# Optimization experiments

Hardware: AMD Instinct MI355X
Metric: run time of the kernel (lower is better)

The kernel has to match this reference:

```python
import jax, jax.numpy as jnp
import numpy as np

N_QUBITS = 10
N_LAYERS = 2
OUT_FEATURES = 64
N_BATCH = 128


def _apply_ry(state, theta, q, n):
    # state: [B, 2^n] real (RY gates are real), theta: [B]
    B = state.shape[0]
    left = 2 ** q
    right = 2 ** (n - q - 1)
    s = state.reshape(B, left, 2, right)
    half = theta * 0.5
    c = jnp.cos(half)[:, None, None]
    sn = jnp.sin(half)[:, None, None]
    s0 = s[:, :, 0, :]
    s1 = s[:, :, 1, :]
    out = jnp.stack([c * s0 - sn * s1, sn * s0 + c * s1], axis=2)
    return out.reshape(B, -1)


def _apply_cnot(state, q, n):
    # control qubit q, target qubit q+1 (adjacent), real statevector
    B = state.shape[0]
    left = 2 ** q
    right = 2 ** (n - q - 2)
    s = state.reshape(B, left, 2, 2, right)
    flipped = jnp.flip(s[:, :, 1, :, :], axis=2)  # swap target amps where control=1
    out = jnp.stack([s[:, :, 0, :, :], flipped], axis=2)
    return out.reshape(B, -1)


def _zdiag(n):
    # diagonal of H = sum_i Z_i in the computational basis: n - 2*popcount(index)
    idx = np.arange(2 ** n)
    pop = np.array([bin(i).count('1') for i in range(2 ** n)], dtype=np.float32)
    return jnp.asarray(n - 2.0 * pop, dtype=jnp.float32)


def setup_inputs() -> dict:
    key = jax.random.key(0)
    kx, kw = jax.random.split(key)
    x = jax.random.normal(kx, (N_BATCH, N_QUBITS), dtype=jnp.float32)
    weight = jax.random.normal(kw, (OUT_FEATURES, N_QUBITS, N_LAYERS), dtype=jnp.float32)
    return {"x": x, "weight": weight}


def reference(x, weight):
    n_batch, n = x.shape
    out_features, _, n_layers = weight.shape
    B = out_features * n_batch
    # x.repeat(out_features, 1): tile batch across output features
    xb = jnp.tile(x, (out_features, 1))  # [B, n]
    # weight expanded over batch: [O, 1, n, L] -> [O, nb, n, L] -> [B, n, L]
    pb = jnp.broadcast_to(weight[:, None, :, :], (out_features, n_batch, n, n_layers))
    pb = pb.reshape(B, n, n_layers)
    # |0...0> statevector, real since the circuit (RY + CNOT) is real
    state = jnp.zeros((B, 2 ** n), dtype=jnp.float32).at[:, 0].set(1.0)
    # data-encoding layer: RY(x_q) on each qubit
    for q in range(n):
        state = _apply_ry(state, xb[:, q], q, n)
    # variational layers: RY(theta_{q,l}) on each qubit + CNOT ladder entangler
    for l in range(n_layers):
        for q in range(n):
            state = _apply_ry(state, pb[:, q, l], q, n)
        for q in range(n - 1):
            state = _apply_cnot(state, q, n)
    zd = _zdiag(n)
    # energy expectation <psi| sum_i Z_i |psi> (real circuit -> real output)
    out = jnp.einsum('bk,k->b', state * state, zd)  # [B]
    return out.reshape(out_features, n_batch)
```

## Files before the change

kernel.cpp:

```cpp
#include <hip/hip_runtime.h>
#include <math.h>


__global__ __launch_bounds__(128) void qnn_closed_v14(const float* gx,
                                                      const float* gw,
                                                      float* gout) {
    __shared__ float wc0[10], ws0[10], wc1[10], ws1[10];
    const int b = (int)threadIdx.x;
    const int f = (int)blockIdx.x;

    if (b < 20) {
        const int q = b % 10;
        const int l = b / 10;
        const float a = gw[(f * 10 + q) * 2 + l];
        if (l == 0) { wc0[q] = cosf(a); ws0[q] = sinf(a); }
        else        { wc1[q] = cosf(a); ws1[q] = sinf(a); }
    }
    __syncthreads();

    float z[10], xv[10], cc[10], ss[10];
    #pragma unroll
    for (int q = 0; q < 10; ++q) {
        const float xa = gx[b * 10 + q];
        const float cx = cosf(xa), sx = sinf(xa);
        z[q]  = cx * wc0[q] - sx * ws0[q];
        xv[q] = sx * wc0[q] + cx * ws0[q];
        cc[q] = wc1[q];
        ss[q] = ws1[q];
    }

    float E = 0.0f;
    #pragma unroll
    for (int k = 0; k < 10; ++k) {
        float v00 = cc[k];
        float v10 = -ss[k] * ((k < 9) ? xv[k + 1] : 1.0f);
        float v01 = 0.0f, v11 = 0.0f;
        #pragma unroll
        for (int j = k - 1; j >= 0; --j) {
            const float zj = z[j + 1], xj = xv[j + 1];
            const float n00 =  cc[j] * (v01 + xj * v10);
            const float n01 =  cc[j] * (zj * v00);
            const float n10 = -ss[j] * (xj * v01 + v10);
            const float n11 = -ss[j] * (zj * v11);
            v00 = n00; v01 = n01; v10 = n10; v11 = n11;
        }
        E += v00 * z[0] + v01 + v10 * xv[0];
    }

    gout[f * 128 + b] = E;
}

extern "C" void kernel_launch(void* const* d_in, const int* in_sizes, int n_in,
                              void* d_out, int out_size, void* d_ws, size_t ws_size,
                              hipStream_t stream) {
    const float* x = (const float*)d_in[0];
    const float* w = (const float*)d_in[1];
    float* out = (float*)d_out;

    hipLaunchKernelGGL(qnn_closed_v14, dim3(64), dim3(128), 0, stream, x, w, out);
}
```

Measured before the change: 56.90 us.

## Collapse nested transfer recurrence into linear pass and use fast sincos

Replaces the quadratic nested loop over qubit pairs with a single forward recurrence carrying three running terms that accumulate the energy. Uses __sincosf intrinsics instead of separate precise cosf/sinf calls and loads each row of x as float2 vectors. This cuts arithmetic and transcendental cost per thread, at the price of lower trigonometric accuracy from the fast intrinsics.

```diff
diff --git a/kernel.cpp b/kernel.cpp
--- a/kernel.cpp
+++ b/kernel.cpp
@@ -2,9 +2,9 @@
 #include <math.h>
 
 
-__global__ __launch_bounds__(128) void qnn_closed_v14(const float* gx,
-                                                      const float* gw,
-                                                      float* gout) {
+__global__ __launch_bounds__(128) void qnn_closed_v15(const float* __restrict__ gx,
+                                                      const float* __restrict__ gw,
+                                                      float* __restrict__ gout) {
     __shared__ float wc0[10], ws0[10], wc1[10], ws1[10];
     const int b = (int)threadIdx.x;
     const int f = (int)blockIdx.x;
@@ -13,38 +13,51 @@
         const int q = b % 10;
         const int l = b / 10;
         const float a = gw[(f * 10 + q) * 2 + l];
-        if (l == 0) { wc0[q] = cosf(a); ws0[q] = sinf(a); }
-        else        { wc1[q] = cosf(a); ws1[q] = sinf(a); }
+        float s, c;
+        __sincosf(a, &s, &c);
+        if (l == 0) { wc0[q] = c; ws0[q] = s; }
+        else        { wc1[q] = c; ws1[q] = s; }
     }
     __syncthreads();
 
-    float z[10], xv[10], cc[10], ss[10];
+    float xa[10];
+    {
+        const float2* gx2 = reinterpret_cast<const float2*>(gx + b * 10);
+        #pragma unroll
+        for (int i = 0; i < 5; ++i) {
+            const float2 v = gx2[i];
+            xa[2 * i]     = v.x;
+            xa[2 * i + 1] = v.y;
+        }
+    }
+
+    float z[10], xv[10];
     #pragma unroll
     for (int q = 0; q < 10; ++q) {
-        const float xa = gx[b * 10 + q];
-        const float cx = cosf(xa), sx = sinf(xa);
+        float sx, cx;
+        __sincosf(xa[q], &sx, &cx);
         z[q]  = cx * wc0[q] - sx * ws0[q];
         xv[q] = sx * wc0[q] + cx * ws0[q];
-        cc[q] = wc1[q];
-        ss[q] = ws1[q];
     }
 
+    float r0 = z[0], r1 = 1.0f, r2 = xv[0];
     float E = 0.0f;
     #pragma unroll
     for (int k = 0; k < 10; ++k) {
-        float v00 = cc[k];
-        float v10 = -ss[k] * ((k < 9) ? xv[k + 1] : 1.0f);
-        float v01 = 0.0f, v11 = 0.0f;
-        #pragma unroll
-        for (int j = k - 1; j >= 0; --j) {
-            const float zj = z[j + 1], xj = xv[j + 1];
-            const float n00 =  cc[j] * (v01 + xj * v10);
-            const float n01 =  cc[j] * (zj * v00);
-            const float n10 = -ss[j] * (xj * v01 + v10);
-            const float n11 = -ss[j] * (zj * v11);
-            v00 = n00; v01 = n01; v10 = n10; v11 = n11;
+        const float cck = wc1[k];
+        const float ssk = ws1[k];
+        const float fk = (k < 9) ? xv[k + 1] : 1.0f;
+        E += cck * r0 - ssk * fk * r2;
+        if (k < 9) {
+            const float zk = z[k + 1];
+            const float xk = xv[k + 1];
+            const float t  = cck * r0;
+            const float u  = ssk * r2;
+            const float n0 = cck * zk * r1;
+            r1 = t - xk * u;
+            r2 = xk * t - u;
+            r0 = n0;
         }
-        E += v00 * z[0] + v01 + v10 * xv[0];
     }
 
     gout[f * 128 + b] = E;
@@ -57,5 +70,5 @@
     const float* w = (const float*)d_in[1];
     float* out = (float*)d_out;
 
-    hipLaunchKernelGGL(qnn_closed_v14, dim3(64), dim3(128), 0, stream, x, w, out);
+    hipLaunchKernelGGL(qnn_closed_v15, dim3(64), dim3(128), 0, stream, x, w, out);
 }
```

After: 54.70 us. 3.9% less time.
